# Kernel optimization log

Hardware: AMD Instinct MI355X
Metric: run time of the kernel (lower is better)

The kernel has to match this reference:

```python
import jax, jax.numpy as jnp
import numpy as np

COLOR_SIZE = 8
FILTERS = 64
LAYERS = 4
CUMSUM_NORM = 256 * 256 * 3  # hardcoded in original: /256/256/3


def setup_inputs() -> dict:
    key = jax.random.key(0)
    k0, k1, k2, k3 = jax.random.split(key, 4)
    s = 0.05
    example = jax.random.randint(k0, (4, 256, 256, 3), 0, COLOR_SIZE, dtype=jnp.int32)
    # per-channel Dense stacks: layer 0 has input dim 1, layers 1..3 have input dim FILTERS
    W_in_first = jax.random.normal(k1, (3, 1, FILTERS), dtype=jnp.float32) * s
    b_in_first = jnp.zeros((3, FILTERS), dtype=jnp.float32)
    W_in_rest = jax.random.normal(k2, (LAYERS - 1, 3, FILTERS, FILTERS), dtype=jnp.float32) * s
    b_in_rest = jnp.zeros((LAYERS - 1, 3, FILTERS), dtype=jnp.float32)
    W_final = jax.random.normal(k3, (3, FILTERS, COLOR_SIZE), dtype=jnp.float32) * s
    b_final = jnp.zeros((3, COLOR_SIZE), dtype=jnp.float32)
    return {
        "example": example,
        "W_in_first": W_in_first, "b_in_first": b_in_first,
        "W_in_rest": W_in_rest, "b_in_rest": b_in_rest,
        "W_final": W_final, "b_final": b_final,
    }


def reference(example, W_in_first, b_in_first, W_in_rest, b_in_rest, W_final, b_final):
    # example: [B, H, W, 3] int in [0, COLOR_SIZE)
    x = example.astype(jnp.float32) / COLOR_SIZE * 2.0 - 1.0
    B, H, W, _ = x.shape
    L = H * W
    x = x.reshape(B, L, 3, 1)

    def layer(x, Wl, bl):
        # per-channel dense + relu: [B, L, 3, din] x [3, din, dout] -> [B, L, 3, dout]
        x = jax.nn.relu(jnp.einsum('blcd,cde->blce', x, Wl) + bl)
        # flatten channels into the sequence and take causal running sum
        x = x.reshape(B, L * 3, FILTERS)
        x = jnp.cumsum(x, axis=-2) / CUMSUM_NORM
        return x.reshape(B, L, 3, FILTERS)

    x = layer(x, W_in_first, b_in_first)
    for i in range(LAYERS - 1):
        x = layer(x, W_in_rest[i], b_in_rest[i])

    # final per-channel dense to color logits (no activation)
    x = jnp.einsum('blcd,cde->blce', x, W_final) + b_final
    return x.reshape(B, H, W, 3, COLOR_SIZE)
```

## Files before the change

### kernel.cpp

```cpp
#include <hip/hip_runtime.h>
#include <stdint.h>


#define BB 4
#define SP 65536
#define SS 196608
#define CI 1024
#define NG 16
#define INVN (1.0f / 196608.0f)

typedef __attribute__((ext_vector_type(8))) _Float16 half8;
typedef __attribute__((ext_vector_type(4))) float    f32x4;

__global__ __launch_bounds__(256)
void prep(const int* __restrict__ ex, const float* __restrict__ W0,
          const float* __restrict__ b0, const float* __restrict__ Wr,
          const float* __restrict__ Wfin,
          _Float16* __restrict__ Wt16, _Float16* __restrict__ Wf16p,
          float* __restrict__ Wf32, float* __restrict__ tab32,
          int* __restrict__ Hsub, int* __restrict__ Hqrt,
          float* __restrict__ Gz)
{
    __shared__ int hist[16][24];
    int tid = threadIdx.x, bi = blockIdx.x;
    int b = bi >> 6, g = (bi >> 2) & 15, q = bi & 3;
    for (int i = tid; i < 384; i += 256) hist[i / 24][i % 24] = 0;
    __syncthreads();
    for (int it = 0; it < 4; ++it) {
        int pl = it * 256 + tid;
        const int* ep = ex + ((size_t)b * SP + g * 4096 + q * 1024 + pl) * 3;
        int j = pl >> 6;
        atomicAdd(&hist[j][ep[0]], 1);
        atomicAdd(&hist[j][8 + ep[1]], 1);
        atomicAdd(&hist[j][16 + ep[2]], 1);
    }
    __syncthreads();
    for (int i = tid; i < 384; i += 256) {
        int j = i / 24, cv = i % 24;
        Hsub[(size_t)(b * CI + g * 64 + q * 16 + j) * 24 + cv] = hist[j][cv];
    }
    if (tid < 24) {
        int s = 0;
        for (int j = 0; j < 16; ++j) s += hist[j][tid];
        Hqrt[((size_t)(b * NG + g) * 4 + q) * 24 + tid] = s;
    }
    {
        int i0 = bi * 256 + tid, nth = 256 * 256;
        for (int idx = i0; idx < 12288; idx += nth)
            Gz[idx] = 0.f;
        for (int idx = i0; idx < 36864; idx += nth) {
            int d = idx & 63, f = (idx >> 6) & 63, lc = idx >> 12;
            Wt16[idx] = (_Float16)Wr[(size_t)(lc * 64 + d) * 64 + f];
        }
        for (int idx = i0; idx < 3072; idx += nth) {
            int d = idx & 63, n = (idx >> 6) & 15, c = idx >> 10;
            Wf16p[idx] = (n < 8) ? (_Float16)Wfin[(size_t)(c * 64 + d) * 8 + n]
                                 : (_Float16)0.f;
        }
        for (int idx = i0; idx < 1536; idx += nth) {
            int d = idx & 63, ck = idx >> 6;
            Wf32[idx] = Wfin[(size_t)((ck >> 3) * 64 + d) * 8 + (ck & 7)];
        }
        for (int idx = i0; idx < 1536; idx += nth) {
            int f = idx & 63, v = (idx >> 6) & 7, c = idx >> 9;
            float xv = v * 0.25f - 1.0f;
            tab32[idx] = fmaxf(W0[c * 64 + f] * xv + b0[c * 64 + f], 0.f);
        }
    }
}

__global__ __launch_bounds__(256, 4)
void midA(const int* __restrict__ ex,
          const int* __restrict__ Hsub, const int* __restrict__ Hqrt,
          const float* __restrict__ tab32,
          const _Float16* __restrict__ W16, const float* __restrict__ Wd32,
          const float* __restrict__ bias, _Float16* __restrict__ Y,
          float* __restrict__ A64, float* __restrict__ Ggrp)
{
    __shared__ float stab[1536];
    __shared__ __align__(16) _Float16 bounce3[3][64 * 72];
    __shared__ float segwt[3][4][64];
    __shared__ float basearr[192];
    __shared__ float hpart[4][24];
    __shared__ float carry[64];

    int tid = threadIdx.x, bi = blockIdx.x;
    int b = bi >> 10, ci = bi & 1023, g = ci >> 6, cr = ci & 63;
    int w = tid >> 6, ln = tid & 63, lm = ln & 15, lq = ln >> 4;
    int P0 = ci * 64;

    for (int i = tid; i < 1536; i += 256) stab[i] = tab32[i];
    if (ln < 24) {
        float s = 0.f;
        for (int j = w; j < g; j += 4) {
            const int* hq = Hqrt + ((size_t)(b * NG + j) * 4) * 24 + ln;
            s += (float)(hq[0] + hq[24] + hq[48] + hq[72]);
        }
        const int* hp = Hsub + (size_t)(b * CI + g * 64) * 24 + ln;
        for (int j = w; j < cr; j += 4) s += (float)hp[j * 24];
        hpart[w][ln] = s;
    }
    __syncthreads();

    float y0[3][16];
    {
#pragma unroll
        for (int p = 0; p < 16; ++p) {
            const int* ep = ex + ((size_t)b * SP + P0 + w * 16 + p) * 3;
            y0[0][p] = stab[ep[0] * 64 + ln];
            y0[1][p] = stab[(8 + ep[1]) * 64 + ln];
            y0[2][p] = stab[(16 + ep[2]) * 64 + ln];
        }
#pragma unroll
        for (int c = 0; c < 3; ++c)
#pragma unroll
            for (int p = 1; p < 16; ++p) y0[c][p] += y0[c][p - 1];
#pragma unroll
        for (int c = 0; c < 3; ++c) segwt[c][w][ln] = y0[c][15];
    }
    if (tid < 64) {
        float c0 = 0.f;
#pragma unroll
        for (int cv = 0; cv < 24; ++cv) {
            float cnt = hpart[0][cv] + hpart[1][cv] + hpart[2][cv] + hpart[3][cv];
            c0 += cnt * stab[cv * 64 + tid];
        }
        carry[tid] = c0;
    }
    __syncthreads();

    {
        float off0[3];
#pragma unroll
        for (int c = 0; c < 3; ++c) {
            float o = 0.f;
            for (int w2 = 0; w2 < w; ++w2) o += segwt[c][w2][ln];
            off0[c] = o;
        }
#pragma unroll
        for (int p = 0; p < 16; ++p) {
            float S0 = y0[0][p] + off0[0], S1 = y0[1][p] + off0[1], S2 = y0[2][p] + off0[2];
            float P1 = p ? y0[1][p - 1] + off0[1] : off0[1];
            float P2 = p ? y0[2][p - 1] + off0[2] : off0[2];
            int row = w * 16 + p;
            bounce3[0][row * 72 + ln] = (_Float16)(S0 + P1 + P2);
            bounce3[1][row * 72 + ln] = (_Float16)(S0 + S1 + P2);
            bounce3[2][row * 72 + ln] = (_Float16)(S0 + S1 + S2);
        }
    }
    if (tid < 192) {
        int c = tid >> 6, f = tid & 63;
        const float* wp = Wd32 + (size_t)(c * 64) * 64 + f;
        float a = 0.f;
        for (int d = 0; d < 64; ++d) a += carry[d] * wp[d * 64];
        basearr[tid] = bias[tid] + INVN * a;
    }
    __syncthreads();

    f32x4 acc[3][4];
#pragma unroll
    for (int c = 0; c < 3; ++c) {
        const half8* bb = (const half8*)&bounce3[c][0];
        half8 a0 = bb[(w * 16 + lm) * 9 + lq];
        half8 a1 = bb[(w * 16 + lm) * 9 + 4 + lq];
#pragma unroll
        for (int nt = 0; nt < 4; ++nt) {
            const half8* bp = (const half8*)(W16 + (size_t)(c * 64 + nt * 16 + lm) * 64);
            f32x4 t = {0.f, 0.f, 0.f, 0.f};
            t = __builtin_amdgcn_mfma_f32_16x16x32_f16(a0, bp[lq],     t, 0, 0, 0);
            t = __builtin_amdgcn_mfma_f32_16x16x32_f16(a1, bp[4 + lq], t, 0, 0, 0);
            acc[c][nt] = t;
        }
    }

    float s[3][4][4], wexcl[3][4];
#pragma unroll
    for (int c = 0; c < 3; ++c)
#pragma unroll
        for (int nt = 0; nt < 4; ++nt) {
            float base = basearr[c * 64 + nt * 16 + lm];
            float run = 0.f;
#pragma unroll
            for (int r = 0; r < 4; ++r) {
                float yv = fmaxf(base + INVN * acc[c][nt][r], 0.f);
                run += yv; s[c][nt][r] = run;
            }
            float v = run;
            float t1 = __shfl_up(v, 16); if (lq >= 1) v += t1;
            float t2 = __shfl_up(v, 32); if (lq >= 2) v += t2;
            wexcl[c][nt] = v - run;
            if (lq == 3) segwt[c][w][nt * 16 + lm] = v;
        }
    __syncthreads();

    {
        float off[3][4], tot[3][4];
#pragma unroll
        for (int c = 0; c < 3; ++c)
#pragma unroll
            for (int nt = 0; nt < 4; ++nt) {
                float o = wexcl[c][nt], ts = 0.f;
#pragma unroll
                for (int w2 = 0; w2 < 4; ++w2) {
                    float wv = segwt[c][w2][nt * 16 + lm];
                    ts += wv;
                    if (w2 < w) o += wv;
                }
                off[c][nt] = o; tot[c][nt] = ts;
            }
        if (w == 0 && lq == 0)
#pragma unroll
            for (int nt = 0; nt < 4; ++nt) {
                float t3 = tot[0][nt] + tot[1][nt] + tot[2][nt];
                A64[(size_t)(b * CI + ci) * 64 + nt * 16 + lm] = t3;
                atomicAdd(&Ggrp[(size_t)(b * NG + g) * 64 + nt * 16 + lm], t3);
            }
#pragma unroll
        for (int nt = 0; nt < 4; ++nt)
#pragma unroll
            for (int r = 0; r < 4; ++r) {
                float S0 = off[0][nt] + s[0][nt][r];
                float S1 = off[1][nt] + s[1][nt][r];
                float S2 = off[2][nt] + s[2][nt][r];
                float P1 = off[1][nt] + (r ? s[1][nt][r - 1] : 0.f);
                float P2 = off[2][nt] + (r ? s[2][nt][r - 1] : 0.f);
                int row = w * 16 + lq * 4 + r;
                bounce3[0][row * 72 + nt * 16 + lm] = (_Float16)(S0 + P1 + P2);
                bounce3[1][row * 72 + nt * 16 + lm] = (_Float16)(S0 + S1 + P2);
                bounce3[2][row * 72 + nt * 16 + lm] = (_Float16)(S0 + S1 + S2);
            }
    }
    __syncthreads();
#pragma unroll
    for (int q = 0; q < 6; ++q) {
        int idx = q * 256 + tid;
        int c = idx >> 9, rem = idx & 511;
        int pix = rem >> 3, f8 = rem & 7;
        half8 v = *(const half8*)&bounce3[c][pix * 72 + f8 * 8];
        ((half8*)(Y + ((size_t)(b * 3 + c) * SP + P0 + pix) * 64))[f8] = v;
    }
}

__global__ __launch_bounds__(256, 4)
void midB(const _Float16* Yin, _Float16* Yout,
          const float* __restrict__ A64p, const float* __restrict__ Ggrp_p,
          const _Float16* __restrict__ W16, const float* __restrict__ Wd32,
          const float* __restrict__ bias,
          float* __restrict__ A64, float* __restrict__ Ggrp)
{
    __shared__ __align__(16) _Float16 bounce3[3][64 * 72];
    __shared__ float wtop[3][4][64];
    __shared__ float basearr[192];
    __shared__ float cpart[4][64];
    __shared__ float carry[64];

    int tid = threadIdx.x, bi = blockIdx.x;
    int b = bi >> 10, ci = bi & 1023, g = ci >> 6, cr = ci & 63;
    int w = tid >> 6, ln = tid & 63, lm = ln & 15, lq = ln >> 4;
    int P0 = ci * 64;

    half8 af0[3], af1[3];
#pragma unroll
    for (int c = 0; c < 3; ++c) {
        const half8* ap = (const half8*)(Yin + ((size_t)(b * 3 + c) * SP + P0 + w * 16 + lm) * 64);
        af0[c] = ap[lq]; af1[c] = ap[4 + lq];
    }
    {
        float s = 0.f;
        for (int j = w; j < g; j += 4)
            s += Ggrp_p[(size_t)(b * NG + j) * 64 + ln];
        const float* ap = A64p + (size_t)(b * CI + g * 64) * 64 + ln;
        for (int j = w; j < cr; j += 4) s += ap[j * 64];
        cpart[w][ln] = s;
    }
    __syncthreads();
    if (tid < 64)
        carry[tid] = cpart[0][tid] + cpart[1][tid] + cpart[2][tid] + cpart[3][tid];
    __syncthreads();
    if (tid < 192) {
        int c = tid >> 6, f = tid & 63;
        const float* wp = Wd32 + (size_t)(c * 64) * 64 + f;
        float a = 0.f;
        for (int d = 0; d < 64; ++d) a += carry[d] * wp[d * 64];
        basearr[tid] = bias[tid] + INVN * a;
    }
    __syncthreads();

    f32x4 acc[3][4];
#pragma unroll
    for (int c = 0; c < 3; ++c)
#pragma unroll
        for (int nt = 0; nt < 4; ++nt) {
            const half8* bp = (const half8*)(W16 + (size_t)(c * 64 + nt * 16 + lm) * 64);
            f32x4 t = {0.f, 0.f, 0.f, 0.f};
            t = __builtin_amdgcn_mfma_f32_16x16x32_f16(af0[c], bp[lq],     t, 0, 0, 0);
            t = __builtin_amdgcn_mfma_f32_16x16x32_f16(af1[c], bp[4 + lq], t, 0, 0, 0);
            acc[c][nt] = t;
        }

    float s[3][4][4], wexcl[3][4];
#pragma unroll
    for (int c = 0; c < 3; ++c)
#pragma unroll
        for (int nt = 0; nt < 4; ++nt) {
            float base = basearr[c * 64 + nt * 16 + lm];
            float run = 0.f;
#pragma unroll
            for (int r = 0; r < 4; ++r) {
                float yv = fmaxf(base + INVN * acc[c][nt][r], 0.f);
                run += yv; s[c][nt][r] = run;
            }
            float v = run;
            float t1 = __shfl_up(v, 16); if (lq >= 1) v += t1;
            float t2 = __shfl_up(v, 32); if (lq >= 2) v += t2;
            wexcl[c][nt] = v - run;
            if (lq == 3) wtop[c][w][nt * 16 + lm] = v;
        }
    __syncthreads();

    {
        float off[3][4], tot[3][4];
#pragma unroll
        for (int c = 0; c < 3; ++c)
#pragma unroll
            for (int nt = 0; nt < 4; ++nt) {
                float o = wexcl[c][nt], ts = 0.f;
#pragma unroll
                for (int w2 = 0; w2 < 4; ++w2) {
                    float wv = wtop[c][w2][nt * 16 + lm];
                    ts += wv;
                    if (w2 < w) o += wv;
                }
                off[c][nt] = o; tot[c][nt] = ts;
            }
        if (w == 0 && lq == 0)
#pragma unroll
            for (int nt = 0; nt < 4; ++nt) {
                float t3 = tot[0][nt] + tot[1][nt] + tot[2][nt];
                A64[(size_t)(b * CI + ci) * 64 + nt * 16 + lm] = t3;
                atomicAdd(&Ggrp[(size_t)(b * NG + g) * 64 + nt * 16 + lm], t3);
            }
#pragma unroll
        for (int nt = 0; nt < 4; ++nt)
#pragma unroll
            for (int r = 0; r < 4; ++r) {
                float S0 = off[0][nt] + s[0][nt][r];
                float S1 = off[1][nt] + s[1][nt][r];
                float S2 = off[2][nt] + s[2][nt][r];
                float P1 = off[1][nt] + (r ? s[1][nt][r - 1] : 0.f);
                float P2 = off[2][nt] + (r ? s[2][nt][r - 1] : 0.f);
                int row = w * 16 + lq * 4 + r;
                bounce3[0][row * 72 + nt * 16 + lm] = (_Float16)(S0 + P1 + P2);
                bounce3[1][row * 72 + nt * 16 + lm] = (_Float16)(S0 + S1 + P2);
                bounce3[2][row * 72 + nt * 16 + lm] = (_Float16)(S0 + S1 + S2);
            }
    }
    __syncthreads();
#pragma unroll
    for (int q = 0; q < 6; ++q) {
        int idx = q * 256 + tid;
        int c = idx >> 9, rem = idx & 511;
        int pix = rem >> 3, f8 = rem & 7;
        half8 v = *(const half8*)&bounce3[c][pix * 72 + f8 * 8];
        ((half8*)(Yout + ((size_t)(b * 3 + c) * SP + P0 + pix) * 64))[f8] = v;
    }
}

__global__ __launch_bounds__(256, 4)
void midC(const _Float16* __restrict__ Yin,
          const float* __restrict__ A64p, const float* __restrict__ Ggrp_p,
          const _Float16* __restrict__ W16, const float* __restrict__ Wd32,
          const float* __restrict__ bias,
          const _Float16* __restrict__ Wf16p, const float* __restrict__ bfin,
          float* __restrict__ out, float* __restrict__ A64, float* __restrict__ Ggrp)
{
    __shared__ __align__(16) _Float16 bounce3[3][64 * 72];
    __shared__ float wtop[3][4][64];
    __shared__ float basearr[192];
    __shared__ float cpart[4][64];
    __shared__ float carry[64];
    __shared__ __align__(16) float outst[64 * 28];

    int tid = threadIdx.x, bi = blockIdx.x;
    int b = bi >> 10, ci = bi & 1023, g = ci >> 6, cr = ci & 63;
    int w = tid >> 6, ln = tid & 63, lm = ln & 15, lq = ln >> 4;
    int P0 = ci * 64;

    half8 af0[3], af1[3];
#pragma unroll
    for (int c = 0; c < 3; ++c) {
        const half8* ap = (const half8*)(Yin + ((size_t)(b * 3 + c) * SP + P0 + w * 16 + lm) * 64);
        af0[c] = ap[lq]; af1[c] = ap[4 + lq];
    }
    {
        float s = 0.f;
        for (int j = w; j < g; j += 4)
            s += Ggrp_p[(size_t)(b * NG + j) * 64 + ln];
        const float* ap = A64p + (size_t)(b * CI + g * 64) * 64 + ln;
        for (int j = w; j < cr; j += 4) s += ap[j * 64];
        cpart[w][ln] = s;
    }
    __syncthreads();
    if (tid < 64)
        carry[tid] = cpart[0][tid] + cpart[1][tid] + cpart[2][tid] + cpart[3][tid];
    __syncthreads();
    if (tid < 192) {
        int c = tid >> 6, f = tid & 63;
        const float* wp = Wd32 + (size_t)(c * 64) * 64 + f;
        float a = 0.f;
        for (int d = 0; d < 64; ++d) a += carry[d] * wp[d * 64];
        basearr[tid] = bias[tid] + INVN * a;
    }
    __syncthreads();

    f32x4 acc[3][4];
#pragma unroll
    for (int c = 0; c < 3; ++c)
#pragma unroll
        for (int nt = 0; nt < 4; ++nt) {
            const half8* bp = (const half8*)(W16 + (size_t)(c * 64 + nt * 16 + lm) * 64);
            f32x4 t = {0.f, 0.f, 0.f, 0.f};
            t = __builtin_amdgcn_mfma_f32_16x16x32_f16(af0[c], bp[lq],     t, 0, 0, 0);
            t = __builtin_amdgcn_mfma_f32_16x16x32_f16(af1[c], bp[4 + lq], t, 0, 0, 0);
            acc[c][nt] = t;
        }

    float s[3][4][4], wexcl[3][4];
#pragma unroll
    for (int c = 0; c < 3; ++c)
#pragma unroll
        for (int nt = 0; nt < 4; ++nt) {
            float base = basearr[c * 64 + nt * 16 + lm];
            float run = 0.f;
#pragma unroll
            for (int r = 0; r < 4; ++r) {
                float yv = fmaxf(base + INVN * acc[c][nt][r], 0.f);
                run += yv; s[c][nt][r] = run;
            }
            float v = run;
            float t1 = __shfl_up(v, 16); if (lq >= 1) v += t1;
            float t2 = __shfl_up(v, 32); if (lq >= 2) v += t2;
            wexcl[c][nt] = v - run;
            if (lq == 3) wtop[c][w][nt * 16 + lm] = v;
        }
    __syncthreads();

    {
        float off[3][4], tot[3][4];
#pragma unroll
        for (int c = 0; c < 3; ++c)
#pragma unroll
            for (int nt = 0; nt < 4; ++nt) {
                float o = wexcl[c][nt], ts = 0.f;
#pragma unroll
                for (int w2 = 0; w2 < 4; ++w2) {
                    float wv = wtop[c][w2][nt * 16 + lm];
                    ts += wv;
                    if (w2 < w) o += wv;
                }
                off[c][nt] = o; tot[c][nt] = ts;
            }
        if (w == 0 && lq == 0)
#pragma unroll
            for (int nt = 0; nt < 4; ++nt) {
                float t3 = tot[0][nt] + tot[1][nt] + tot[2][nt];
                A64[(size_t)(b * CI + ci) * 64 + nt * 16 + lm] = t3;
                atomicAdd(&Ggrp[(size_t)(b * NG + g) * 64 + nt * 16 + lm], t3);
            }
#pragma unroll
        for (int nt = 0; nt < 4; ++nt)
#pragma unroll
            for (int r = 0; r < 4; ++r) {
                float S0 = off[0][nt] + s[0][nt][r];
                float S1 = off[1][nt] + s[1][nt][r];
                float S2 = off[2][nt] + s[2][nt][r];
                float P1 = off[1][nt] + (r ? s[1][nt][r - 1] : 0.f);
                float P2 = off[2][nt] + (r ? s[2][nt][r - 1] : 0.f);
                int row = w * 16 + lq * 4 + r;
                bounce3[0][row * 72 + nt * 16 + lm] = (_Float16)(S0 + P1 + P2);
                bounce3[1][row * 72 + nt * 16 + lm] = (_Float16)(S0 + S1 + P2);
                bounce3[2][row * 72 + nt * 16 + lm] = (_Float16)(S0 + S1 + S2);
            }
    }
    __syncthreads();

#pragma unroll
    for (int c = 0; c < 3; ++c) {
        const half8* bb = (const half8*)&bounce3[c][0];
        half8 fa0 = bb[(w * 16 + lm) * 9 + lq];
        half8 fa1 = bb[(w * 16 + lm) * 9 + 4 + lq];
        const half8* fb = (const half8*)(Wf16p + (size_t)(c * 16 + lm) * 64);
        f32x4 t = {0.f, 0.f, 0.f, 0.f};
        t = __builtin_amdgcn_mfma_f32_16x16x32_f16(fa0, fb[lq],     t, 0, 0, 0);
        t = __builtin_amdgcn_mfma_f32_16x16x32_f16(fa1, fb[4 + lq], t, 0, 0, 0);
        if (lm < 8) {
            float bz = bfin[c * 8 + lm];
#pragma unroll
            for (int r = 0; r < 4; ++r)
                outst[(w * 16 + lq * 4 + r) * 28 + c * 8 + lm] = bz + INVN * t[r];
        }
    }
    __syncthreads();
    {
        float4* obase = (float4*)(out + ((size_t)b * SS + (size_t)P0 * 3) * 8);
#pragma unroll
        for (int k = 0; k < 2; ++k) {
            int idx = k * 256 + tid;
            if (idx < 384) {
                int pix = idx / 6, sub = (idx % 6) * 4;
                obase[idx] = *(const float4*)&outst[pix * 28 + sub];
            }
        }
    }
}

__global__ __launch_bounds__(256, 4)
void fixk(const float* __restrict__ A64p, const float* __restrict__ Ggrp_p,
          const float* __restrict__ Wf32, float* __restrict__ out)
{
    __shared__ float cpart[4][64];
    __shared__ float carry[64];
    __shared__ float part[24][8];
    __shared__ float vfix[24];
    int tid = threadIdx.x, bi = blockIdx.x;
    int b = bi >> 10, ci = bi & 1023, g = ci >> 6, cr = ci & 63;
    int w = tid >> 6, ln = tid & 63;
    int P0 = ci * 64;

    {
        float s = 0.f;
        for (int j = w; j < g; j += 4)
            s += Ggrp_p[(size_t)(b * NG + j) * 64 + ln];
        const float* ap = A64p + (size_t)(b * CI + g * 64) * 64 + ln;
        for (int j = w; j < cr; j += 4) s += ap[j * 64];
        cpart[w][ln] = s;
    }
    __syncthreads();
    if (tid < 64)
        carry[tid] = cpart[0][tid] + cpart[1][tid] + cpart[2][tid] + cpart[3][tid];
    __syncthreads();
    if (tid < 192) {
        int ck = tid >> 3, sg = tid & 7;
        const float* wp = Wf32 + ck * 64 + sg * 8;
        const float* cp = carry + sg * 8;
        float vf = 0.f;
#pragma unroll
        for (int d = 0; d < 8; ++d) vf += cp[d] * wp[d];
        part[ck][sg] = vf;
    }
    __syncthreads();
    if (tid < 24) {
        float vf = 0.f;
#pragma unroll
        for (int j = 0; j < 8; ++j) vf += part[tid][j];
        vfix[tid] = INVN * vf;
    }
    __syncthreads();
    float4* obase = (float4*)(out + ((size_t)b * SS + (size_t)P0 * 3) * 8);
#pragma unroll
    for (int k = 0; k < 2; ++k) {
        int idx = k * 256 + tid;
        if (idx < 384) {
            int sub = (idx % 6) * 4;
            float4 v = obase[idx];
            v.x += vfix[sub];
            v.y += vfix[sub + 1];
            v.z += vfix[sub + 2];
            v.w += vfix[sub + 3];
            obase[idx] = v;
        }
    }
}

extern "C" void kernel_launch(void* const* d_in, const int* in_sizes, int n_in,
                              void* d_out, int out_size, void* d_ws, size_t ws_size,
                              hipStream_t stream)
{
    const int*   ex   = (const int*)d_in[0];
    const float* W0   = (const float*)d_in[1];
    const float* b0   = (const float*)d_in[2];
    const float* Wr   = (const float*)d_in[3];
    const float* br   = (const float*)d_in[4];
    const float* Wfin = (const float*)d_in[5];
    const float* bfin = (const float*)d_in[6];
    float* out = (float*)d_out;

    char* ws = (char*)d_ws;
    size_t off = 0;
    _Float16* Y = (_Float16*)(ws + off); off += (size_t)BB * 3 * SP * 64 * 2;
    float* Ggrp1 = (float*)(ws + off); off += (size_t)BB * NG * 64 * 4;
    float* Ggrp2 = (float*)(ws + off); off += (size_t)BB * NG * 64 * 4;
    float* Ggrp3 = (float*)(ws + off); off += (size_t)BB * NG * 64 * 4;
    float* A64_1 = (float*)(ws + off); off += (size_t)BB * CI * 64 * 4;
    float* A64_2 = (float*)(ws + off); off += (size_t)BB * CI * 64 * 4;
    float* A64_3 = (float*)(ws + off); off += (size_t)BB * CI * 64 * 4;
    int* Hsub = (int*)(ws + off); off += (size_t)BB * CI * 24 * 4;
    int* Hqrt = (int*)(ws + off); off += (size_t)BB * NG * 4 * 24 * 4;
    _Float16* Wt16  = (_Float16*)(ws + off); off += 36864 * 2;
    _Float16* Wf16p = (_Float16*)(ws + off); off += 3072 * 2;
    float* Wf32  = (float*)(ws + off); off += 1536 * 4;
    float* tab32 = (float*)(ws + off); off += 1536 * 4;

    prep<<<256, 256, 0, stream>>>(ex, W0, b0, Wr, Wfin,
                                  Wt16, Wf16p, Wf32, tab32,
                                  Hsub, Hqrt, Ggrp1);
    midA<<<4096, 256, 0, stream>>>(ex, Hsub, Hqrt, tab32,
                                   Wt16, Wr, br, Y, A64_1, Ggrp1);
    midB<<<4096, 256, 0, stream>>>(Y, Y, A64_1, Ggrp1,
                                   Wt16 + 12288, Wr + 12288, br + 192,
                                   A64_2, Ggrp2);
    midC<<<4096, 256, 0, stream>>>(Y, A64_2, Ggrp2,
                                   Wt16 + 24576, Wr + 24576, br + 384,
                                   Wf16p, bfin, out, A64_3, Ggrp3);
    fixk<<<4096, 256, 0, stream>>>(A64_3, Ggrp3, Wf32, out);
}
```

Baseline: 358.6 us.

## Precompute per-chunk carry bias in separate kernels before each mid layer

Moves the per-chunk prefix-carry reduction and the carry-times-weight matvec out of midA/midB/midC into small carry kernels. These compute all 1024 chunk base vectors per batch with a running scan and weights held in LDS. Each mid block previously redid an O(chunk index) serial reduction over earlier chunks plus a 64x64 matvec. The mid kernels now just load 192 precomputed floats. The cost is three extra launches with only 64 blocks each, which serialize between layers, plus about 9 MB of extra workspace traffic.

```diff
diff --git a/kernel.cpp b/kernel.cpp
--- a/kernel.cpp
+++ b/kernel.cpp
@@ -69,37 +69,125 @@
     }
 }
 
+__global__ __launch_bounds__(768)
+void carryk1(const int* __restrict__ Hsub, const int* __restrict__ Hqrt,
+             const float* __restrict__ tab32, const float* __restrict__ W,
+             const float* __restrict__ bias, float* __restrict__ Bout)
+{
+    __shared__ float WL[12288];
+    __shared__ float tabL[1536];
+    __shared__ float cp[64][24];
+    __shared__ float car[64][64];
+    int tid = threadIdx.x, bi = blockIdx.x;
+    int b = bi >> 4, g = bi & 15;
+    int ci0 = g * 64;
+
+    for (int i = tid; i < 12288; i += 768) WL[i] = W[i];
+    for (int i = tid; i < 1536; i += 768) tabL[i] = tab32[i];
+    if (tid < 24) {
+        float run = 0.f;
+        for (int j = 0; j < g; ++j) {
+            const int* hq = Hqrt + ((size_t)(b * NG + j) * 4) * 24 + tid;
+            run += (float)(hq[0] + hq[24] + hq[48] + hq[72]);
+        }
+        const int* hp = Hsub + (size_t)(b * CI + ci0) * 24 + tid;
+        for (int j = 0; j < 64; ++j) { cp[j][tid] = run; run += (float)hp[j * 24]; }
+    }
+    __syncthreads();
+    {
+        int jj = tid >> 6, f = tid & 63;
+        for (int p = 0; p < 6; ++p) {
+            int j = p * 12 + jj;
+            if (j < 64) {
+                float a = 0.f;
+#pragma unroll
+                for (int cv = 0; cv < 24; ++cv)
+                    a = fmaf(cp[j][cv], tabL[cv * 64 + f], a);
+                car[j][f] = a;
+            }
+        }
+    }
+    __syncthreads();
+    {
+        int sub = tid / 192, o = tid - sub * 192;
+        int c = o >> 6, fo = o & 63;
+        const float* wl = &WL[c * 4096 + fo];
+        float bz = bias[o];
+        for (int p = 0; p < 16; ++p) {
+            int cj = p * 4 + sub;
+            float a = 0.f;
+#pragma unroll 16
+            for (int d = 0; d < 64; ++d)
+                a = fmaf(car[cj][d], wl[d * 64], a);
+            Bout[(size_t)(b * CI + ci0 + cj) * 192 + o] = bz + INVN * a;
+        }
+    }
+}
+
+__global__ __launch_bounds__(768)
+void carryk(const float* __restrict__ A64p, const float* __restrict__ Ggrp_p,
+            const float* __restrict__ W, const float* __restrict__ bias,
+            float* __restrict__ Bout)
+{
+    __shared__ float WL[12288];
+    __shared__ float a64[64][64];
+    __shared__ float car[64][64];
+    __shared__ float gp[64];
+    int tid = threadIdx.x, bi = blockIdx.x;
+    int b = bi >> 4, g = bi & 15;
+    int ci0 = g * 64;
+
+    for (int i = tid; i < 12288; i += 768) WL[i] = W[i];
+    for (int i = tid; i < 4096; i += 768) {
+        int j = i >> 6, f = i & 63;
+        a64[j][f] = A64p[(size_t)(b * CI + ci0 + j) * 64 + f];
+    }
+    if (tid < 64) {
+        float s = 0.f;
+        for (int j = 0; j < g; ++j)
+            s += Ggrp_p[(size_t)(b * NG + j) * 64 + tid];
+        gp[tid] = s;
+    }
+    __syncthreads();
+    if (tid < 64) {
+        float run = gp[tid];
+        for (int j = 0; j < 64; ++j) { car[j][tid] = run; run += a64[j][tid]; }
+    }
+    __syncthreads();
+    {
+        int sub = tid / 192, o = tid - sub * 192;
+        int c = o >> 6, fo = o & 63;
+        const float* wl = &WL[c * 4096 + fo];
+        float bz = bias[o];
+        for (int p = 0; p < 16; ++p) {
+            int cj = p * 4 + sub;
+            float a = 0.f;
+#pragma unroll 16
+            for (int d = 0; d < 64; ++d)
+                a = fmaf(car[cj][d], wl[d * 64], a);
+            Bout[(size_t)(b * CI + ci0 + cj) * 192 + o] = bz + INVN * a;
+        }
+    }
+}
+
 __global__ __launch_bounds__(256, 4)
-void midA(const int* __restrict__ ex,
-          const int* __restrict__ Hsub, const int* __restrict__ Hqrt,
-          const float* __restrict__ tab32,
-          const _Float16* __restrict__ W16, const float* __restrict__ Wd32,
-          const float* __restrict__ bias, _Float16* __restrict__ Y,
+void midA(const int* __restrict__ ex, const float* __restrict__ tab32,
+          const _Float16* __restrict__ W16, const float* __restrict__ B1p,
+          _Float16* __restrict__ Y,
           float* __restrict__ A64, float* __restrict__ Ggrp)
 {
     __shared__ float stab[1536];
     __shared__ __align__(16) _Float16 bounce3[3][64 * 72];
     __shared__ float segwt[3][4][64];
     __shared__ float basearr[192];
-    __shared__ float hpart[4][24];
-    __shared__ float carry[64];
 
     int tid = threadIdx.x, bi = blockIdx.x;
-    int b = bi >> 10, ci = bi & 1023, g = ci >> 6, cr = ci & 63;
+    int b = bi >> 10, ci = bi & 1023, g = ci >> 6;
     int w = tid >> 6, ln = tid & 63, lm = ln & 15, lq = ln >> 4;
     int P0 = ci * 64;
 
     for (int i = tid; i < 1536; i += 256) stab[i] = tab32[i];
-    if (ln < 24) {
-        float s = 0.f;
-        for (int j = w; j < g; j += 4) {
-            const int* hq = Hqrt + ((size_t)(b * NG + j) * 4) * 24 + ln;
-            s += (float)(hq[0] + hq[24] + hq[48] + hq[72]);
-        }
-        const int* hp = Hsub + (size_t)(b * CI + g * 64) * 24 + ln;
-        for (int j = w; j < cr; j += 4) s += (float)hp[j * 24];
-        hpart[w][ln] = s;
-    }
+    if (tid < 192) basearr[tid] = B1p[(size_t)(b * CI + ci) * 192 + tid];
     __syncthreads();
 
     float y0[3][16];
@@ -117,15 +205,6 @@
             for (int p = 1; p < 16; ++p) y0[c][p] += y0[c][p - 1];
 #pragma unroll
         for (int c = 0; c < 3; ++c) segwt[c][w][ln] = y0[c][15];
-    }
-    if (tid < 64) {
-        float c0 = 0.f;
-#pragma unroll
-        for (int cv = 0; cv < 24; ++cv) {
-            float cnt = hpart[0][cv] + hpart[1][cv] + hpart[2][cv] + hpart[3][cv];
-            c0 += cnt * stab[cv * 64 + tid];
-        }
-        carry[tid] = c0;
     }
     __syncthreads();
 
@@ -147,13 +226,6 @@
             bounce3[1][row * 72 + ln] = (_Float16)(S0 + S1 + P2);
             bounce3[2][row * 72 + ln] = (_Float16)(S0 + S1 + S2);
         }
-    }
-    if (tid < 192) {
-        int c = tid >> 6, f = tid & 63;
-        const float* wp = Wd32 + (size_t)(c * 64) * 64 + f;
-        float a = 0.f;
-        for (int d = 0; d < 64; ++d) a += carry[d] * wp[d * 64];
-        basearr[tid] = bias[tid] + INVN * a;
     }
     __syncthreads();
 
@@ -242,20 +314,16 @@
 }
 
 __global__ __launch_bounds__(256, 4)
-void midB(const _Float16* Yin, _Float16* Yout,
-          const float* __restrict__ A64p, const float* __restrict__ Ggrp_p,
-          const _Float16* __restrict__ W16, const float* __restrict__ Wd32,
-          const float* __restrict__ bias,
+void midB(const _Float16* Yin, _Float16* Yout, const float* __restrict__ B2p,
+          const _Float16* __restrict__ W16,
           float* __restrict__ A64, float* __restrict__ Ggrp)
 {
     __shared__ __align__(16) _Float16 bounce3[3][64 * 72];
     __shared__ float wtop[3][4][64];
     __shared__ float basearr[192];
-    __shared__ float cpart[4][64];
-    __shared__ float carry[64];
 
     int tid = threadIdx.x, bi = blockIdx.x;
-    int b = bi >> 10, ci = bi & 1023, g = ci >> 6, cr = ci & 63;
+    int b = bi >> 10, ci = bi & 1023, g = ci >> 6;
     int w = tid >> 6, ln = tid & 63, lm = ln & 15, lq = ln >> 4;
     int P0 = ci * 64;
 
@@ -265,25 +333,7 @@
         const half8* ap = (const half8*)(Yin + ((size_t)(b * 3 + c) * SP + P0 + w * 16 + lm) * 64);
         af0[c] = ap[lq]; af1[c] = ap[4 + lq];
     }
-    {
-        float s = 0.f;
-        for (int j = w; j < g; j += 4)
-            s += Ggrp_p[(size_t)(b * NG + j) * 64 + ln];
-        const float* ap = A64p + (size_t)(b * CI + g * 64) * 64 + ln;
-        for (int j = w; j < cr; j += 4) s += ap[j * 64];
-        cpart[w][ln] = s;
-    }
-    __syncthreads();
-    if (tid < 64)
-        carry[tid] = cpart[0][tid] + cpart[1][tid] + cpart[2][tid] + cpart[3][tid];
-    __syncthreads();
-    if (tid < 192) {
-        int c = tid >> 6, f = tid & 63;
-        const float* wp = Wd32 + (size_t)(c * 64) * 64 + f;
-        float a = 0.f;
-        for (int d = 0; d < 64; ++d) a += carry[d] * wp[d * 64];
-        basearr[tid] = bias[tid] + INVN * a;
-    }
+    if (tid < 192) basearr[tid] = B2p[(size_t)(b * CI + ci) * 192 + tid];
     __syncthreads();
 
     f32x4 acc[3][4];
@@ -367,22 +417,18 @@
 }
 
 __global__ __launch_bounds__(256, 4)
-void midC(const _Float16* __restrict__ Yin,
-          const float* __restrict__ A64p, const float* __restrict__ Ggrp_p,
-          const _Float16* __restrict__ W16, const float* __restrict__ Wd32,
-          const float* __restrict__ bias,
+void midC(const _Float16* __restrict__ Yin, const float* __restrict__ B3p,
+          const _Float16* __restrict__ W16,
           const _Float16* __restrict__ Wf16p, const float* __restrict__ bfin,
           float* __restrict__ out, float* __restrict__ A64, float* __restrict__ Ggrp)
 {
     __shared__ __align__(16) _Float16 bounce3[3][64 * 72];
     __shared__ float wtop[3][4][64];
     __shared__ float basearr[192];
-    __shared__ float cpart[4][64];
-    __shared__ float carry[64];
     __shared__ __align__(16) float outst[64 * 28];
 
     int tid = threadIdx.x, bi = blockIdx.x;
-    int b = bi >> 10, ci = bi & 1023, g = ci >> 6, cr = ci & 63;
+    int b = bi >> 10, ci = bi & 1023, g = ci >> 6;
     int w = tid >> 6, ln = tid & 63, lm = ln & 15, lq = ln >> 4;
     int P0 = ci * 64;
 
@@ -392,25 +438,7 @@
         const half8* ap = (const half8*)(Yin + ((size_t)(b * 3 + c) * SP + P0 + w * 16 + lm) * 64);
         af0[c] = ap[lq]; af1[c] = ap[4 + lq];
     }
-    {
-        float s = 0.f;
-        for (int j = w; j < g; j += 4)
-            s += Ggrp_p[(size_t)(b * NG + j) * 64 + ln];
-        const float* ap = A64p + (size_t)(b * CI + g * 64) * 64 + ln;
-        for (int j = w; j < cr; j += 4) s += ap[j * 64];
-        cpart[w][ln] = s;
-    }
-    __syncthreads();
-    if (tid < 64)
-        carry[tid] = cpart[0][tid] + cpart[1][tid] + cpart[2][tid] + cpart[3][tid];
-    __syncthreads();
-    if (tid < 192) {
-        int c = tid >> 6, f = tid & 63;
-        const float* wp = Wd32 + (size_t)(c * 64) * 64 + f;
-        float a = 0.f;
-        for (int d = 0; d < 64; ++d) a += carry[d] * wp[d * 64];
-        basearr[tid] = bias[tid] + INVN * a;
-    }
+    if (tid < 192) basearr[tid] = B3p[(size_t)(b * CI + ci) * 192 + tid];
     __syncthreads();
 
     f32x4 acc[3][4];
@@ -596,6 +624,9 @@
     float* A64_3 = (float*)(ws + off); off += (size_t)BB * CI * 64 * 4;
     int* Hsub = (int*)(ws + off); off += (size_t)BB * CI * 24 * 4;
     int* Hqrt = (int*)(ws + off); off += (size_t)BB * NG * 4 * 24 * 4;
+    float* B1a = (float*)(ws + off); off += (size_t)BB * CI * 192 * 4;
+    float* B2a = (float*)(ws + off); off += (size_t)BB * CI * 192 * 4;
+    float* B3a = (float*)(ws + off); off += (size_t)BB * CI * 192 * 4;
     _Float16* Wt16  = (_Float16*)(ws + off); off += 36864 * 2;
     _Float16* Wf16p = (_Float16*)(ws + off); off += 3072 * 2;
     float* Wf32  = (float*)(ws + off); off += 1536 * 4;
@@ -604,13 +635,12 @@
     prep<<<256, 256, 0, stream>>>(ex, W0, b0, Wr, Wfin,
                                   Wt16, Wf16p, Wf32, tab32,
                                   Hsub, Hqrt, Ggrp1);
-    midA<<<4096, 256, 0, stream>>>(ex, Hsub, Hqrt, tab32,
-                                   Wt16, Wr, br, Y, A64_1, Ggrp1);
-    midB<<<4096, 256, 0, stream>>>(Y, Y, A64_1, Ggrp1,
-                                   Wt16 + 12288, Wr + 12288, br + 192,
-                                   A64_2, Ggrp2);
-    midC<<<4096, 256, 0, stream>>>(Y, A64_2, Ggrp2,
-                                   Wt16 + 24576, Wr + 24576, br + 384,
-                                   Wf16p, bfin, out, A64_3, Ggrp3);
+    carryk1<<<64, 768, 0, stream>>>(Hsub, Hqrt, tab32, Wr, br, B1a);
+    midA<<<4096, 256, 0, stream>>>(ex, tab32, Wt16, B1a, Y, A64_1, Ggrp1);
+    carryk<<<64, 768, 0, stream>>>(A64_1, Ggrp1, Wr + 12288, br + 192, B2a);
+    midB<<<4096, 256, 0, stream>>>(Y, Y, B2a, Wt16 + 12288, A64_2, Ggrp2);
+    carryk<<<64, 768, 0, stream>>>(A64_2, Ggrp2, Wr + 24576, br + 384, B3a);
+    midC<<<4096, 256, 0, stream>>>(Y, B3a, Wt16 + 24576, Wf16p, bfin,
+                                   out, A64_3, Ggrp3);
     fixk<<<4096, 256, 0, stream>>>(A64_3, Ggrp3, Wf32, out);
 }
```

After: 403.3 us. 12.5% more time.
